# Performance work log

Hardware: AMD Instinct MI355X
Metric: run time of the kernel (lower is better)

## Reference

```python
import jax, jax.numpy as jnp
import numpy as np

S, B, C, H = 1024, 4, 1024, 16
CC = C // H


def setup_inputs() -> dict:
    key = jax.random.key(0)
    ks = jax.random.split(key, 10)
    scale = 1.0 / np.sqrt(C)
    return {
        "x": jax.random.normal(ks[0], (S, B, C), dtype=jnp.float32),
        "r": jax.random.normal(ks[1], (S, B, C), dtype=jnp.float32),
        "Wq": jax.random.normal(ks[2], (C, C), dtype=jnp.float32) * scale,
        "bq": jnp.zeros((C,), dtype=jnp.float32),
        "Wke": jax.random.normal(ks[3], (C, C), dtype=jnp.float32) * scale,
        "bke": jnp.zeros((C,), dtype=jnp.float32),
        "Wkr": jax.random.normal(ks[4], (C, C), dtype=jnp.float32) * scale,
        "bkr": jnp.zeros((C,), dtype=jnp.float32),
        "u": jax.random.normal(ks[5], (C,), dtype=jnp.float32) * 0.02,
        "v": jax.random.normal(ks[6], (C,), dtype=jnp.float32) * 0.02,
    }


def reference(x, r, Wq, bq, Wke, bke, Wkr, bkr, u, v):
    s, b, c = x.shape
    h, cc = H, CC
    # projections (torch Linear: y = x @ W^T + b)
    ewq = (x @ Wq.T + bq).reshape(s, b, h, cc)
    ewke_full = x @ Wke.T + bke                 # [s,b,c]
    ewke = ewke_full.reshape(s, b, h, cc)
    rwkr_full = r @ Wkr.T + bkr                 # [s,b,c]
    rwkr = rwkr_full.reshape(s, b, h, cc)
    # content-content and content-position terms
    term_a = jnp.einsum('sbnc,tbnc->stbn', ewq, ewke)
    term_b = jnp.einsum('sbnc,tbnc->stbn', ewq, rwkr)
    # global bias terms: uwke/vwke are constant over (s,b), so the stb einsum
    # reduces to a tb contraction broadcast over s (same math, no s*b copies)
    uwke = Wke @ u + bke                        # [c]
    vwke = Wkr @ v + bkr                        # [c]
    term_c = jnp.einsum('c,tbc->tb', uwke, ewke_full)   # [t,b]
    term_d = jnp.einsum('c,tbc->tb', vwke, rwkr_full)   # [t,b]
    bias = (term_c + term_d)[None, :, :, None]          # [1,t,b,1]
    return term_a + term_b + bias               # [s,t,b,h]
```

## Files before the change

### kernel.cpp

```cpp
#include <hip/hip_runtime.h>
#include <hip/hip_bf16.h>
#include <stdint.h>

#define Ssz 1024
#define Bsz 4
#define Csz 1024
#define Hsz 16
#define Msz 4096

typedef unsigned short u16;
typedef __attribute__((ext_vector_type(8))) short bf16x8;
typedef __attribute__((ext_vector_type(8))) unsigned short u16x8;
typedef __attribute__((ext_vector_type(4))) float f32x4;
typedef __attribute__((ext_vector_type(4))) unsigned short u16x4;

__device__ __forceinline__ u16 f2bf(float f) {
  union { float f; unsigned u; } x; x.f = f;
  unsigned r = x.u + 0x7fffu + ((x.u >> 16) & 1u);
  return (u16)(r >> 16);
}

__device__ __forceinline__ void glds16(const void* g, void* l) {
  __builtin_amdgcn_global_load_lds(
      (__attribute__((address_space(1))) void*)g,
      (__attribute__((address_space(3))) void*)l, 16, 0, 0);
}

__device__ __forceinline__ int swzb(int x) { return x ^ (((x >> 8) & 7) << 4); }

__global__ __launch_bounds__(256) void k_prep1(
    const float* __restrict__ Wke, const float* __restrict__ bke, const float* __restrict__ uu,
    const float* __restrict__ Wkr, const float* __restrict__ bkr, const float* __restrict__ vv,
    float* __restrict__ uwke, float* __restrict__ vwke) {
  int w = blockIdx.x * 4 + (threadIdx.x >> 6);
  int lane = threadIdx.x & 63;
  const float* Wrow; const float* vec; const float* bias; float* outp; int c;
  if (w < 1024) { c = w;        Wrow = Wke + (size_t)c * Csz; vec = uu; bias = bke; outp = uwke; }
  else          { c = w - 1024; Wrow = Wkr + (size_t)c * Csz; vec = vv; bias = bkr; outp = vwke; }
  float s = 0.f;
  const float4* W4 = (const float4*)Wrow;
  const float4* V4 = (const float4*)vec;
  #pragma unroll
  for (int i = lane; i < 256; i += 64) {
    float4 a = W4[i], b = V4[i];
    s += a.x * b.x + a.y * b.y + a.z * b.z + a.w * b.w;
  }
  for (int m = 32; m; m >>= 1) s += __shfl_xor(s, m);
  if (lane == 0) outp[c] = s + bias[c];
}

__global__ __launch_bounds__(256) void k_prep2(
    const float* __restrict__ Wke, const float* __restrict__ Wkr,
    const float* __restrict__ uwke, const float* __restrict__ vwke,
    const float* __restrict__ bke, const float* __restrict__ bkr,
    float* __restrict__ wu, float* __restrict__ wv, float* __restrict__ cst) {
  int bid = blockIdx.x;
  int tid = threadIdx.x;
  if (bid < 64) {
    const float* W = (bid < 32) ? Wke : Wkr;
    const float* sv = (bid < 32) ? uwke : vwke;
    float* o = (bid < 32) ? wu : wv;
    int d = (bid & 31) * 32 + (tid & 31);
    int cpar = tid >> 5;
    float acc = 0.f;
    #pragma unroll 8
    for (int c = cpar; c < Csz; c += 8) acc += sv[c] * W[(size_t)c * Csz + d];
    __shared__ float red[8][32];
    red[cpar][tid & 31] = acc;
    __syncthreads();
    if (cpar == 0) {
      float s = 0.f;
      #pragma unroll
      for (int i = 0; i < 8; i++) s += red[i][tid & 31];
      o[d] = s;
    }
  } else {
    float s = 0.f;
    for (int i = tid; i < Csz; i += 256) s += uwke[i] * bke[i] + vwke[i] * bkr[i];
    for (int m = 32; m; m >>= 1) s += __shfl_xor(s, m);
    __shared__ float red1[4];
    if ((tid & 63) == 0) red1[tid >> 6] = s;
    __syncthreads();
    if (tid == 0) cst[0] = red1[0] + red1[1] + red1[2] + red1[3];
  }
}

__global__ __launch_bounds__(256) void k_convert_xr(
    const float* __restrict__ x, const float* __restrict__ r, u16* __restrict__ A2) {
  int g = blockIdx.x * 256 + threadIdx.x;
  int m = g >> 8;
  int c4 = (g & 255) * 4;
  float4 xv = *(const float4*)(x + (size_t)m * Csz + c4);
  float4 rv = *(const float4*)(r + (size_t)m * Csz + c4);
  u16x4 xo = { f2bf(xv.x), f2bf(xv.y), f2bf(xv.z), f2bf(xv.w) };
  u16x4 ro = { f2bf(rv.x), f2bf(rv.y), f2bf(rv.z), f2bf(rv.w) };
  *(u16x4*)(A2 + (size_t)m * 2048 + c4) = xo;
  *(u16x4*)(A2 + (size_t)m * 2048 + 1024 + c4) = ro;
}

__global__ __launch_bounds__(256) void k_convert_w(
    const float* __restrict__ Wq, const float* __restrict__ Wke, const float* __restrict__ Wkr,
    const float* __restrict__ bke, const float* __restrict__ bkr,
    u16* __restrict__ Bq, u16* __restrict__ B2, float* __restrict__ biasK) {
  int g = blockIdx.x * 256 + threadIdx.x;
  int c = g >> 8;
  int c4 = (g & 255) * 4;
  float4 q = *(const float4*)(Wq + (size_t)c * Csz + c4);
  float4 e = *(const float4*)(Wke + (size_t)c * Csz + c4);
  float4 k = *(const float4*)(Wkr + (size_t)c * Csz + c4);
  u16x4 qo = { f2bf(q.x), f2bf(q.y), f2bf(q.z), f2bf(q.w) };
  u16x4 eo = { f2bf(e.x), f2bf(e.y), f2bf(e.z), f2bf(e.w) };
  u16x4 ko = { f2bf(k.x), f2bf(k.y), f2bf(k.z), f2bf(k.w) };
  *(u16x4*)(Bq + (size_t)c * 1024 + c4) = qo;
  *(u16x4*)(B2 + (size_t)c * 2048 + c4) = eo;
  *(u16x4*)(B2 + (size_t)c * 2048 + 1024 + c4) = ko;
  if (threadIdx.x == 0) biasK[c] = bke[c] + bkr[c];
}

__global__ __launch_bounds__(256) void k_gemm(
    const u16* __restrict__ A2, const u16* __restrict__ Bq, const u16* __restrict__ B2,
    const float* __restrict__ bq, const float* __restrict__ biasK,
    u16* __restrict__ QF, u16* __restrict__ KF) {
  __shared__ u16 As[128 * 32];
  __shared__ u16 Bs[128 * 32];
  __shared__ u16 ep[4][4096];
  const int z = blockIdx.z;
  const u16* A = A2; const int lda = 2048;
  const u16* B = (z == 0) ? Bq : B2;
  const int ldb = (z == 0) ? 1024 : 2048;
  const float* bias = (z == 0) ? bq : biasK;
  u16* OF = (z == 0) ? QF : KF;
  const int K = (z == 0) ? 1024 : 2048;

  const int tid = threadIdx.x;
  const int bm = blockIdx.y * 128, bn = blockIdx.x * 128;
  const int wave = tid >> 6, lane = tid & 63;
  const int wm = (wave & 1) * 64, wn = (wave >> 1) * 64;
  const int fr = lane & 15, kg = (lane >> 4) * 8;

  f32x4 acc[4][4] = {};

  for (int kt = 0; kt < K; kt += 32) {
    __syncthreads();
    #pragma unroll
    for (int i = 0; i < 2; i++) {
      int ch = i * 256 + tid;
      int row = ch >> 2, col = (ch & 3) * 8;
      glds16(A + (size_t)(bm + row) * lda + kt + col, As + ch * 8);
      glds16(B + (size_t)(bn + row) * ldb + kt + col, Bs + ch * 8);
    }
    __syncthreads();
    bf16x8 af[4], bf[4];
    #pragma unroll
    for (int mi = 0; mi < 4; mi++) af[mi] = *(const bf16x8*)(As + (wm + mi * 16 + fr) * 32 + kg);
    #pragma unroll
    for (int ni = 0; ni < 4; ni++) bf[ni] = *(const bf16x8*)(Bs + (wn + ni * 16 + fr) * 32 + kg);
    #pragma unroll
    for (int mi = 0; mi < 4; mi++)
      #pragma unroll
      for (int ni = 0; ni < 4; ni++)
        acc[mi][ni] = __builtin_amdgcn_mfma_f32_16x16x32_bf16(af[mi], bf[ni], acc[mi][ni], 0, 0, 0);
  }

  const int hi = lane >> 4;
  const int e8 = fr & 7;
  const int fr3 = fr >> 3;
  float bvn[4];
  #pragma unroll
  for (int ni = 0; ni < 4; ni++) bvn[ni] = bias[bn + wn + ni * 16 + fr];
  #pragma unroll
  for (int ni = 0; ni < 4; ni++) {
    const int kk = ni >> 1;
    const int g = (ni * 2 + fr3) & 3;
    #pragma unroll
    for (int mi = 0; mi < 4; mi++) {
      const int inner = (g * 16 + mi * 4 + hi) * 8 + e8;
      #pragma unroll
      for (int j = 0; j < 4; j++)
        ep[wave][(j * 2 + kk) * 512 + inner] = f2bf(acc[mi][ni][j] + bvn[ni]);
    }
  }
  const int s_tile = (bm >> 6) + (wm >> 6);
  const int nh = (bn + wn) >> 6;
  #pragma unroll
  for (int p = 0; p < 8; p++) {
    const int b2 = p >> 1, kk = p & 1;
    u16x8 v = *(const u16x8*)(&ep[wave][p * 512 + lane * 8]);
    size_t ci = ((size_t)(s_tile * 4 + b2) * 16 + nh) * 2 + kk;
    *(u16x8*)(OF + ci * 512 + lane * 8) = v;
  }
}

__global__ __launch_bounds__(256) void k_bias(
    const float* __restrict__ x, const float* __restrict__ r,
    const float* __restrict__ wu, const float* __restrict__ wv,
    const float* __restrict__ cst, float* __restrict__ biasTB) {
  int row = blockIdx.x * 4 + (threadIdx.x >> 6);
  int lane = threadIdx.x & 63;
  const float4* xv = (const float4*)(x + (size_t)row * Csz);
  const float4* rv = (const float4*)(r + (size_t)row * Csz);
  const float4* wuv = (const float4*)wu;
  const float4* wvv = (const float4*)wv;
  float s = 0.f;
  #pragma unroll
  for (int i = lane; i < 256; i += 64) {
    float4 a = xv[i], b = wuv[i];
    s += a.x * b.x + a.y * b.y + a.z * b.z + a.w * b.w;
    float4 c = rv[i], d = wvv[i];
    s += c.x * d.x + c.y * d.y + c.z * d.z + c.w * d.w;
  }
  for (int m = 32; m; m >>= 1) s += __shfl_xor(s, m);
  if (lane == 0) biasTB[row] = s + cst[0];
}

__global__ __launch_bounds__(256, 3) void k_attn(
    const u16* __restrict__ QF, const u16* __restrict__ KF,
    const float* __restrict__ biasTB, float* __restrict__ out) {
  int id = blockIdx.x;
  int xcd = id & 7, within = id >> 3;
  int sx = xcd & 3, tx = xcd >> 2;
  int panel = within >> 7;
  int pl = within & 127;
  int s_tile = sx * 16 + (pl >> 3);
  int t_tile = tx * 32 + panel * 8 + (pl & 7);
  int s0 = s_tile * 16, t0 = t_tile * 16;

  int tid = threadIdx.x;
  int wave = tid >> 6, lane = tid & 63;
  int fr = lane & 15;

  const u16* qp = QF + (size_t)(s_tile * 4 + wave) * 16384 + lane * 8;
  const u16* kp = KF + (size_t)(t_tile * 4 + wave) * 16384 + lane * 8;

  f32x4 acc[16];
  #pragma unroll
  for (int n = 0; n < 16; n++) acc[n] = (f32x4){0.f, 0.f, 0.f, 0.f};

  #pragma unroll
  for (int n = 0; n < 16; n++) {
    #pragma unroll
    for (int kk = 0; kk < 2; kk++) {
      bf16x8 a  = *(const bf16x8*)(qp + (n * 2 + kk) * 512);
      bf16x8 bb = *(const bf16x8*)(kp + (n * 2 + kk) * 512);
      acc[n] = __builtin_amdgcn_mfma_f32_16x16x32_bf16(a, bb, acc[n], 0, 0, 0);
    }
  }

  __shared__ float lds[8192];
  float bv = biasTB[(t0 + (tid >> 4)) * 4 + ((tid >> 2) & 3)];
  int hi = (lane >> 4) & 1;
  int myg = (lane >> 4) >> 1;

  #pragma unroll
  for (int g = 0; g < 2; g++) {
    __syncthreads();
    if (myg == g) {
      #pragma unroll
      for (int j = 0; j < 4; j++) {
        int lbase = (((hi * 4 + j) * 16 + fr) * 4 + wave) * 64;
        #pragma unroll
        for (int n0 = 0; n0 < 16; n0 += 4) {
          f32x4 v = { acc[n0][j], acc[n0 + 1][j], acc[n0 + 2][j], acc[n0 + 3][j] };
          *(f32x4*)((char*)lds + swzb(lbase + n0 * 4)) = v;
        }
      }
    }
    __syncthreads();
    #pragma unroll
    for (int sr = 0; sr < 8; sr++) {
      f32x4 v = *(const f32x4*)((char*)lds + swzb(sr * 4096 + tid * 16));
      v += bv;
      size_t off = ((size_t)(s0 + g * 8 + sr) * 1024 + t0) * 64 + tid * 4;
      __builtin_nontemporal_store(v, (f32x4*)(out + off));
    }
  }
}

extern "C" void kernel_launch(void* const* d_in, const int* in_sizes, int n_in,
                              void* d_out, int out_size, void* d_ws, size_t ws_size,
                              hipStream_t stream) {
  const float* x   = (const float*)d_in[0];
  const float* r   = (const float*)d_in[1];
  const float* Wq  = (const float*)d_in[2];
  const float* bq  = (const float*)d_in[3];
  const float* Wke = (const float*)d_in[4];
  const float* bke = (const float*)d_in[5];
  const float* Wkr = (const float*)d_in[6];
  const float* bkr = (const float*)d_in[7];
  const float* uu  = (const float*)d_in[8];
  const float* vv  = (const float*)d_in[9];
  float* out = (float*)d_out;
  char* ws = (char*)d_ws;

  u16* A2 = (u16*)(ws + 0);
  u16* QF = (u16*)(ws + 16777216);
  u16* KF = (u16*)(ws + 25165824);
  u16* B2 = (u16*)(ws + 33554432);
  u16* Bq = (u16*)(ws + 37748736);
  float* uwke  = (float*)(ws + 39845888);
  float* vwke  = (float*)(ws + 39849984);
  float* wu    = (float*)(ws + 39854080);
  float* wv    = (float*)(ws + 39858176);
  float* biasK = (float*)(ws + 39862272);
  float* cst   = (float*)(ws + 39866368);
  float* biasTB = (float*)(ws + 39866624);

  k_prep1<<<512, 256, 0, stream>>>(Wke, bke, uu, Wkr, bkr, vv, uwke, vwke);
  k_prep2<<<65, 256, 0, stream>>>(Wke, Wkr, uwke, vwke, bke, bkr, wu, wv, cst);
  k_convert_xr<<<4096, 256, 0, stream>>>(x, r, A2);
  k_convert_w<<<1024, 256, 0, stream>>>(Wq, Wke, Wkr, bke, bkr, Bq, B2, biasK);
  k_gemm<<<dim3(8, 32, 2), 256, 0, stream>>>(A2, Bq, B2, bq, biasK, QF, KF);
  k_bias<<<1024, 256, 0, stream>>>(x, r, wu, wv, cst, biasTB);
  k_attn<<<4096, 256, 0, stream>>>(QF, KF, biasTB, out);
}
```

Baseline: 150.8 us.

## Fuse prep kernels into conversions, double-buffer GEMM LDS, nontemporal stores

```diff
diff --git a/kernel.cpp b/kernel.cpp
--- a/kernel.cpp
+++ b/kernel.cpp
@@ -28,25 +28,37 @@
 
 __device__ __forceinline__ int swzb(int x) { return x ^ (((x >> 8) & 7) << 4); }
 
-__global__ __launch_bounds__(256) void k_prep1(
-    const float* __restrict__ Wke, const float* __restrict__ bke, const float* __restrict__ uu,
-    const float* __restrict__ Wkr, const float* __restrict__ bkr, const float* __restrict__ vv,
+__global__ __launch_bounds__(256) void k_convert_w(
+    const float* __restrict__ Wq, const float* __restrict__ Wke, const float* __restrict__ Wkr,
+    const float* __restrict__ bke, const float* __restrict__ bkr,
+    const float* __restrict__ uu, const float* __restrict__ vv,
+    u16* __restrict__ Bq, u16* __restrict__ B2, float* __restrict__ biasK,
     float* __restrict__ uwke, float* __restrict__ vwke) {
-  int w = blockIdx.x * 4 + (threadIdx.x >> 6);
-  int lane = threadIdx.x & 63;
-  const float* Wrow; const float* vec; const float* bias; float* outp; int c;
-  if (w < 1024) { c = w;        Wrow = Wke + (size_t)c * Csz; vec = uu; bias = bke; outp = uwke; }
-  else          { c = w - 1024; Wrow = Wkr + (size_t)c * Csz; vec = vv; bias = bkr; outp = vwke; }
-  float s = 0.f;
-  const float4* W4 = (const float4*)Wrow;
-  const float4* V4 = (const float4*)vec;
-  #pragma unroll
-  for (int i = lane; i < 256; i += 64) {
-    float4 a = W4[i], b = V4[i];
-    s += a.x * b.x + a.y * b.y + a.z * b.z + a.w * b.w;
-  }
-  for (int m = 32; m; m >>= 1) s += __shfl_xor(s, m);
-  if (lane == 0) outp[c] = s + bias[c];
+  int c = blockIdx.x;
+  int tid = threadIdx.x;
+  int c4 = tid * 4;
+  float4 q = *(const float4*)(Wq + (size_t)c * Csz + c4);
+  float4 e = *(const float4*)(Wke + (size_t)c * Csz + c4);
+  float4 k = *(const float4*)(Wkr + (size_t)c * Csz + c4);
+  u16x4 qo = { f2bf(q.x), f2bf(q.y), f2bf(q.z), f2bf(q.w) };
+  u16x4 eo = { f2bf(e.x), f2bf(e.y), f2bf(e.z), f2bf(e.w) };
+  u16x4 ko = { f2bf(k.x), f2bf(k.y), f2bf(k.z), f2bf(k.w) };
+  *(u16x4*)(Bq + (size_t)c * 1024 + c4) = qo;
+  *(u16x4*)(B2 + (size_t)c * 2048 + c4) = eo;
+  *(u16x4*)(B2 + (size_t)c * 2048 + 1024 + c4) = ko;
+  float4 u4 = *(const float4*)(uu + c4);
+  float4 v4 = *(const float4*)(vv + c4);
+  float se = e.x * u4.x + e.y * u4.y + e.z * u4.z + e.w * u4.w;
+  float sk = k.x * v4.x + k.y * v4.y + k.z * v4.z + k.w * v4.w;
+  for (int m = 32; m; m >>= 1) { se += __shfl_xor(se, m); sk += __shfl_xor(sk, m); }
+  __shared__ float red[2][4];
+  if ((tid & 63) == 0) { red[0][tid >> 6] = se; red[1][tid >> 6] = sk; }
+  __syncthreads();
+  if (tid == 0) {
+    uwke[c] = red[0][0] + red[0][1] + red[0][2] + red[0][3] + bke[c];
+    vwke[c] = red[1][0] + red[1][1] + red[1][2] + red[1][3] + bkr[c];
+    biasK[c] = bke[c] + bkr[c];
+  }
 }
 
 __global__ __launch_bounds__(256) void k_prep2(
@@ -85,44 +97,36 @@
   }
 }
 
-__global__ __launch_bounds__(256) void k_convert_xr(
-    const float* __restrict__ x, const float* __restrict__ r, u16* __restrict__ A2) {
-  int g = blockIdx.x * 256 + threadIdx.x;
-  int m = g >> 8;
-  int c4 = (g & 255) * 4;
+__global__ __launch_bounds__(256) void k_convert_xr_bias(
+    const float* __restrict__ x, const float* __restrict__ r,
+    const float* __restrict__ wu, const float* __restrict__ wv,
+    const float* __restrict__ cst, u16* __restrict__ A2, float* __restrict__ biasTB) {
+  int m = blockIdx.x;
+  int tid = threadIdx.x;
+  int c4 = tid * 4;
   float4 xv = *(const float4*)(x + (size_t)m * Csz + c4);
   float4 rv = *(const float4*)(r + (size_t)m * Csz + c4);
   u16x4 xo = { f2bf(xv.x), f2bf(xv.y), f2bf(xv.z), f2bf(xv.w) };
   u16x4 ro = { f2bf(rv.x), f2bf(rv.y), f2bf(rv.z), f2bf(rv.w) };
   *(u16x4*)(A2 + (size_t)m * 2048 + c4) = xo;
   *(u16x4*)(A2 + (size_t)m * 2048 + 1024 + c4) = ro;
-}
-
-__global__ __launch_bounds__(256) void k_convert_w(
-    const float* __restrict__ Wq, const float* __restrict__ Wke, const float* __restrict__ Wkr,
-    const float* __restrict__ bke, const float* __restrict__ bkr,
-    u16* __restrict__ Bq, u16* __restrict__ B2, float* __restrict__ biasK) {
-  int g = blockIdx.x * 256 + threadIdx.x;
-  int c = g >> 8;
-  int c4 = (g & 255) * 4;
-  float4 q = *(const float4*)(Wq + (size_t)c * Csz + c4);
-  float4 e = *(const float4*)(Wke + (size_t)c * Csz + c4);
-  float4 k = *(const float4*)(Wkr + (size_t)c * Csz + c4);
-  u16x4 qo = { f2bf(q.x), f2bf(q.y), f2bf(q.z), f2bf(q.w) };
-  u16x4 eo = { f2bf(e.x), f2bf(e.y), f2bf(e.z), f2bf(e.w) };
-  u16x4 ko = { f2bf(k.x), f2bf(k.y), f2bf(k.z), f2bf(k.w) };
-  *(u16x4*)(Bq + (size_t)c * 1024 + c4) = qo;
-  *(u16x4*)(B2 + (size_t)c * 2048 + c4) = eo;
-  *(u16x4*)(B2 + (size_t)c * 2048 + 1024 + c4) = ko;
-  if (threadIdx.x == 0) biasK[c] = bke[c] + bkr[c];
+  float4 a = *(const float4*)(wu + c4);
+  float4 b = *(const float4*)(wv + c4);
+  float s = xv.x * a.x + xv.y * a.y + xv.z * a.z + xv.w * a.w
+          + rv.x * b.x + rv.y * b.y + rv.z * b.z + rv.w * b.w;
+  for (int mm = 32; mm; mm >>= 1) s += __shfl_xor(s, mm);
+  __shared__ float red[4];
+  if ((tid & 63) == 0) red[tid >> 6] = s;
+  __syncthreads();
+  if (tid == 0) biasTB[m] = red[0] + red[1] + red[2] + red[3] + cst[0];
 }
 
 __global__ __launch_bounds__(256) void k_gemm(
     const u16* __restrict__ A2, const u16* __restrict__ Bq, const u16* __restrict__ B2,
     const float* __restrict__ bq, const float* __restrict__ biasK,
     u16* __restrict__ QF, u16* __restrict__ KF) {
-  __shared__ u16 As[128 * 32];
-  __shared__ u16 Bs[128 * 32];
+  __shared__ u16 As[2][4096];
+  __shared__ u16 Bs[2][4096];
   __shared__ u16 ep[4][4096];
   const int z = blockIdx.z;
   const u16* A = A2; const int lda = 2048;
@@ -130,7 +134,7 @@
   const int ldb = (z == 0) ? 1024 : 2048;
   const float* bias = (z == 0) ? bq : biasK;
   u16* OF = (z == 0) ? QF : KF;
-  const int K = (z == 0) ? 1024 : 2048;
+  const int NT = ((z == 0) ? 1024 : 2048) >> 5;
 
   const int tid = threadIdx.x;
   const int bm = blockIdx.y * 128, bn = blockIdx.x * 128;
@@ -138,28 +142,38 @@
   const int wm = (wave & 1) * 64, wn = (wave >> 1) * 64;
   const int fr = lane & 15, kg = (lane >> 4) * 8;
 
+  const int ch0 = tid, ch1 = 256 + tid;
+  const int r0 = ch0 >> 2, c0 = (ch0 & 3) * 8;
+  const int r1 = ch1 >> 2, c1 = (ch1 & 3) * 8;
+  const u16* a0 = A + (size_t)(bm + r0) * lda + c0;
+  const u16* a1 = A + (size_t)(bm + r1) * lda + c1;
+  const u16* b0 = B + (size_t)(bn + r0) * ldb + c0;
+  const u16* b1 = B + (size_t)(bn + r1) * ldb + c1;
+
   f32x4 acc[4][4] = {};
 
-  for (int kt = 0; kt < K; kt += 32) {
-    __syncthreads();
-    #pragma unroll
-    for (int i = 0; i < 2; i++) {
-      int ch = i * 256 + tid;
-      int row = ch >> 2, col = (ch & 3) * 8;
-      glds16(A + (size_t)(bm + row) * lda + kt + col, As + ch * 8);
-      glds16(B + (size_t)(bn + row) * ldb + kt + col, Bs + ch * 8);
-    }
-    __syncthreads();
+  glds16(a0, &As[0][ch0 * 8]);  glds16(a1, &As[0][ch1 * 8]);
+  glds16(b0, &Bs[0][ch0 * 8]);  glds16(b1, &Bs[0][ch1 * 8]);
+  __syncthreads();
+
+  for (int t = 0; t < NT; t++) {
+    const int cur = t & 1;
+    if (t + 1 < NT) {
+      const int kt = (t + 1) * 32;
+      glds16(a0 + kt, &As[cur ^ 1][ch0 * 8]);  glds16(a1 + kt, &As[cur ^ 1][ch1 * 8]);
+      glds16(b0 + kt, &Bs[cur ^ 1][ch0 * 8]);  glds16(b1 + kt, &Bs[cur ^ 1][ch1 * 8]);
+    }
     bf16x8 af[4], bf[4];
     #pragma unroll
-    for (int mi = 0; mi < 4; mi++) af[mi] = *(const bf16x8*)(As + (wm + mi * 16 + fr) * 32 + kg);
-    #pragma unroll
-    for (int ni = 0; ni < 4; ni++) bf[ni] = *(const bf16x8*)(Bs + (wn + ni * 16 + fr) * 32 + kg);
+    for (int mi = 0; mi < 4; mi++) af[mi] = *(const bf16x8*)(&As[cur][(wm + mi * 16 + fr) * 32 + kg]);
+    #pragma unroll
+    for (int ni = 0; ni < 4; ni++) bf[ni] = *(const bf16x8*)(&Bs[cur][(wn + ni * 16 + fr) * 32 + kg]);
     #pragma unroll
     for (int mi = 0; mi < 4; mi++)
       #pragma unroll
       for (int ni = 0; ni < 4; ni++)
         acc[mi][ni] = __builtin_amdgcn_mfma_f32_16x16x32_bf16(af[mi], bf[ni], acc[mi][ni], 0, 0, 0);
+    __syncthreads();
   }
 
   const int hi = lane >> 4;
@@ -187,30 +201,8 @@
     const int b2 = p >> 1, kk = p & 1;
     u16x8 v = *(const u16x8*)(&ep[wave][p * 512 + lane * 8]);
     size_t ci = ((size_t)(s_tile * 4 + b2) * 16 + nh) * 2 + kk;
-    *(u16x8*)(OF + ci * 512 + lane * 8) = v;
-  }
-}
-
-__global__ __launch_bounds__(256) void k_bias(
-    const float* __restrict__ x, const float* __restrict__ r,
-    const float* __restrict__ wu, const float* __restrict__ wv,
-    const float* __restrict__ cst, float* __restrict__ biasTB) {
-  int row = blockIdx.x * 4 + (threadIdx.x >> 6);
-  int lane = threadIdx.x & 63;
-  const float4* xv = (const float4*)(x + (size_t)row * Csz);
-  const float4* rv = (const float4*)(r + (size_t)row * Csz);
-  const float4* wuv = (const float4*)wu;
-  const float4* wvv = (const float4*)wv;
-  float s = 0.f;
-  #pragma unroll
-  for (int i = lane; i < 256; i += 64) {
-    float4 a = xv[i], b = wuv[i];
-    s += a.x * b.x + a.y * b.y + a.z * b.z + a.w * b.w;
-    float4 c = rv[i], d = wvv[i];
-    s += c.x * d.x + c.y * d.y + c.z * d.z + c.w * d.w;
-  }
-  for (int m = 32; m; m >>= 1) s += __shfl_xor(s, m);
-  if (lane == 0) biasTB[row] = s + cst[0];
+    __builtin_nontemporal_store(v, (u16x8*)(OF + ci * 512 + lane * 8));
+  }
 }
 
 __global__ __launch_bounds__(256, 3) void k_attn(
@@ -305,11 +297,10 @@
   float* cst   = (float*)(ws + 39866368);
   float* biasTB = (float*)(ws + 39866624);
 
-  k_prep1<<<512, 256, 0, stream>>>(Wke, bke, uu, Wkr, bkr, vv, uwke, vwke);
+  k_convert_w<<<1024, 256, 0, stream>>>(Wq, Wke, Wkr, bke, bkr, uu, vv,
+                                        Bq, B2, biasK, uwke, vwke);
   k_prep2<<<65, 256, 0, stream>>>(Wke, Wkr, uwke, vwke, bke, bkr, wu, wv, cst);
-  k_convert_xr<<<4096, 256, 0, stream>>>(x, r, A2);
-  k_convert_w<<<1024, 256, 0, stream>>>(Wq, Wke, Wkr, bke, bkr, Bq, B2, biasK);
+  k_convert_xr_bias<<<4096, 256, 0, stream>>>(x, r, wu, wv, cst, A2, biasTB);
   k_gemm<<<dim3(8, 32, 2), 256, 0, stream>>>(A2, Bq, B2, bq, biasK, QF, KF);
-  k_bias<<<1024, 256, 0, stream>>>(x, r, wu, wv, cst, biasTB);
   k_attn<<<4096, 256, 0, stream>>>(QF, KF, biasTB, out);
 }
```

Result: slower. 158.3 us (+5.0%).
